# Kernel tuning notes

Measured on AMD Instinct MI355X. Metric: run time of the kernel, lower is better.

The kernel has to match this reference:

```python
import jax, jax.numpy as jnp
import numpy as np

B, T, D_IN, H = 128, 256, 512, 1024

def setup_inputs() -> dict:
    key = jax.random.key(0)
    ks = jax.random.split(key, 12)
    s = 1.0 / np.sqrt(H)
    return {
        "input": jax.random.normal(ks[0], (B, T, D_IN), jnp.float32),
        "h0": jax.random.normal(ks[1], (B, H), jnp.float32),
        "c0": jax.random.normal(ks[2], (B, H), jnp.float32),
        "ctx": jax.random.normal(ks[3], (B, T, H), jnp.float32),
        "srcmask": jax.random.randint(ks[4], (B, T), 0, 2).astype(bool),
        "W_ih": jax.random.uniform(ks[5], (4 * H, D_IN), jnp.float32, -s, s),
        "W_hh": jax.random.uniform(ks[6], (4 * H, H), jnp.float32, -s, s),
        "b_ih": jax.random.uniform(ks[7], (4 * H,), jnp.float32, -s, s),
        "b_hh": jax.random.uniform(ks[8], (4 * H,), jnp.float32, -s, s),
        "W_attn": jax.random.uniform(ks[9], (H, H), jnp.float32, -s, s),
        "W_out": jax.random.uniform(ks[10], (H, 2 * H), jnp.float32, -s, s),
    }


def reference(input, h0, c0, ctx, srcmask, W_ih, W_hh, b_ih, b_hh, W_attn, W_out):
    def step(carry, x_t):
        h, c = carry
        # LSTMCell: gate order i, f, g, o (PyTorch convention)
        gates = x_t @ W_ih.T + b_ih + h @ W_hh.T + b_hh  # [B, 4H]
        i_g, f_g, g_g, o_g = jnp.split(gates, 4, axis=-1)
        cy = jax.nn.sigmoid(f_g) * c + jax.nn.sigmoid(i_g) * jnp.tanh(g_g)
        hy = jax.nn.sigmoid(o_g) * jnp.tanh(cy)
        # Bilinear attention: score(K_j, q) = K_j^T (W_attn q)
        q = hy @ W_attn.T                                   # [B, H]
        scores = jnp.einsum("blh,bh->bl", ctx, q)          # [B, L]
        scores = jnp.where(srcmask, -jnp.inf, scores)
        probs = jax.nn.softmax(scores, axis=-1)
        wctx = jnp.einsum("bl,blh->bh", probs, ctx)        # [B, H]
        h_tilde = jnp.tanh(jnp.concatenate([wctx, hy], axis=-1) @ W_out.T)
        return (h_tilde, cy), h_tilde

    xs = jnp.transpose(input, (1, 0, 2))  # [T, B, D_IN]
    (h_f, c_f), outs = jax.lax.scan(step, (h0, c0), xs)
    output = jnp.transpose(outs, (1, 0, 2))  # [B, T, H]
    return (output, h_f, c_f)
```

## Files before the change

kernel.cpp:

```cpp
#include <hip/hip_runtime.h>
#include <hip/hip_bf16.h>
#include <math.h>

#define B_  128
#define T_  256
#define DIN 512
#define H_  1024

typedef __attribute__((ext_vector_type(8))) short bf16x8;
typedef __attribute__((ext_vector_type(4))) float f32x4;

#define GLD_LDS16(gsrc, ldst) \
  __builtin_amdgcn_global_load_lds((const __attribute__((address_space(1))) void*)(gsrc), \
                                   (__attribute__((address_space(3))) void*)(ldst), 16, 0, 0)

#define WAITVM_(n) asm volatile("s_waitcnt vmcnt(" #n ")" ::: "memory")
#define WAITVM(n) WAITVM_(n)

__device__ __forceinline__ void split_bf16(float v, __hip_bfloat16* hi, __hip_bfloat16* lo) {
    __hip_bfloat16 h = __float2bfloat16(v);
    *hi = h;
    *lo = __float2bfloat16(v - __bfloat162float(h));
}

__device__ __forceinline__ float sigmoidf_(float x) { return 1.f / (1.f + expf(-x)); }

__global__ void bsum_perm_k(const float* __restrict__ bi, const float* __restrict__ bh,
                            float* __restrict__ o) {
    int c = blockIdx.x * 256 + threadIdx.x;
    int srow = ((c & 3) << 10) | (c >> 2);
    o[c] = bi[srow] + bh[srow];
}

__global__ void detect_mask_k(const int* __restrict__ m, int nwords, int* __restrict__ flag) {
    __shared__ int bad;
    if (threadIdx.x == 0) bad = 0;
    __syncthreads();
    for (int i = threadIdx.x; i < nwords; i += blockDim.x) {
        unsigned v = (unsigned)m[i];
        if (v > 1u) bad = 1;
    }
    __syncthreads();
    if (threadIdx.x == 0) flag[0] = bad ? 0 : 1;
}

__global__ void cvt_split_k(const float* __restrict__ s, __hip_bfloat16* __restrict__ hi,
                            __hip_bfloat16* __restrict__ lo, int n) {
    int i = blockIdx.x * 256 + threadIdx.x;
    if (i < n) split_bf16(s[i], hi + i, lo + i);
}

__global__ void wgp_split_k(const float* __restrict__ Wih, const float* __restrict__ Whh,
                            __hip_bfloat16* __restrict__ Wh, __hip_bfloat16* __restrict__ Wl) {
    long i = (long)blockIdx.x * 256 + threadIdx.x;
    int c = (int)(i / 1536), k = (int)(i - (long)c * 1536);
    int srow = ((c & 3) << 10) | (c >> 2);
    float v = (k < DIN) ? Wih[(long)srow * DIN + k] : Whh[(long)srow * H_ + (k - DIN)];
    split_bf16(v, Wh + i, Wl + i);
}

__global__ void cvtx_k(const float* __restrict__ xsrc, __hip_bfloat16* __restrict__ xh,
                       __hip_bfloat16* __restrict__ xl) {
    int i = blockIdx.x * 256 + threadIdx.x;
    int b = i >> 9, c = i & 511;
    split_bf16(xsrc[(long)b * (T_ * DIN) + c], xh + i, xl + i);
}

constexpr int APL = 128 * 64 * 2;
constexpr int BPL = 32 * 64 * 2;
constexpr int BUFB = 2 * APL + 2 * BPL;
constexpr int LDSZ = 3 * BUFB;

#define GEMM_CORE(NT, NW2, BNV, VMID, NB, KSP, A1H, A1L, LDA1, K1V, A2H, A2L, LDA2, WHP, WLP, LDW) \
    const int n0_ = (NB) * (BNV); \
    const int kbase_ = (KSP) * ((NT) * 64); \
    const int wm_ = (NW2) ? (w >> 1) * 64 : w * 32; \
    const int wn_ = (NW2) ? (w & 1) * 16 : 0; \
    auto stage = [&](int buf, int kt) { \
        char* base = lds + buf * BUFB; \
        const int kb = kbase_ + kt * 64; \
        _Pragma("unroll") \
        for (int pp = 0; pp < 2; ++pp) { \
            const __hip_bfloat16* A1 = pp ? (A1L) : (A1H); \
            const __hip_bfloat16* A2 = pp ? (A2L) : (A2H); \
            _Pragma("unroll") \
            for (int j = 0; j < 4; ++j) { \
                int c = j * 256 + tid; \
                int row = c >> 3, sl2 = c & 7; \
                int e = kb + ((sl2 ^ (row & 7)) << 3); \
                const __hip_bfloat16* src = (e < (K1V)) ? (A1 + (long)row * (LDA1) + e) \
                                                        : (A2 + (long)row * (LDA2) + (e - (K1V))); \
                GLD_LDS16(src, base + pp * APL + ((j * 256 + (tid & 192)) << 4)); \
            } \
            if (tid < (BNV) * 8) { \
                int row = tid >> 3, sl2 = tid & 7; \
                int e = kb + ((sl2 ^ (row & 7)) << 3); \
                const __hip_bfloat16* src = (pp ? (WLP) : (WHP)) + (long)(n0_ + row) * (LDW) + e; \
                GLD_LDS16(src, base + 2 * APL + pp * BPL + ((tid & 192) << 4)); \
            } \
        } \
    }; \
    f32x4 acc[4] = {}; \
    stage(0, 0); \
    if ((NT) > 1) stage(1, 1); \
    for (int kt = 0; kt < (NT); ++kt) { \
        if (kt + 1 < (NT)) { WAITVM(VMID); } else { WAITVM(0); } \
        __builtin_amdgcn_s_barrier(); \
        __builtin_amdgcn_sched_barrier(0); \
        if (kt + 2 < (NT)) stage((kt + 2) % 3, kt + 2); \
        const char* base = lds + (kt % 3) * BUFB; \
        _Pragma("unroll") \
        for (int ks = 0; ks < 2; ++ks) { \
            bf16x8 afh[4], afl[4], bh, bl; \
            _Pragma("unroll") \
            for (int mi = 0; mi < ((NW2) ? 4 : 2); ++mi) { \
                int row = wm_ + mi * 16 + (l & 15); \
                int sl2 = (l >> 4) + ks * 4; \
                int off = row * 128 + ((sl2 ^ (row & 7)) << 4); \
                afh[mi] = *(const bf16x8*)(base + off); \
                afl[mi] = *(const bf16x8*)(base + APL + off); \
            } \
            { \
                int row = wn_ + (l & 15); \
                int sl2 = (l >> 4) + ks * 4; \
                int off = row * 128 + ((sl2 ^ (row & 7)) << 4); \
                bh = *(const bf16x8*)(base + 2 * APL + off); \
                bl = *(const bf16x8*)(base + 2 * APL + BPL + off); \
            } \
            _Pragma("unroll") \
            for (int mi = 0; mi < ((NW2) ? 4 : 2); ++mi) { \
                acc[mi] = __builtin_amdgcn_mfma_f32_16x16x32_bf16(afh[mi], bh, acc[mi], 0, 0, 0); \
                acc[mi] = __builtin_amdgcn_mfma_f32_16x16x32_bf16(afl[mi], bh, acc[mi], 0, 0, 0); \
                acc[mi] = __builtin_amdgcn_mfma_f32_16x16x32_bf16(afh[mi], bl, acc[mi], 0, 0, 0); \
            } \
        } \
    }

__global__ __launch_bounds__(256)
void gemm_g_k(const __hip_bfloat16* __restrict__ xh, const __hip_bfloat16* __restrict__ xl,
              const __hip_bfloat16* __restrict__ hh, const __hip_bfloat16* __restrict__ hl,
              const __hip_bfloat16* __restrict__ Wgh, const __hip_bfloat16* __restrict__ Wgl,
              const float* __restrict__ bsump, float* __restrict__ cbuf,
              __hip_bfloat16* __restrict__ AoBh, __hip_bfloat16* __restrict__ AoBl,
              float* __restrict__ cf,
              const float* __restrict__ input, int t,
              __hip_bfloat16* __restrict__ nxh, __hip_bfloat16* __restrict__ nxl)
{
    __shared__ __attribute__((aligned(16))) char lds[LDSZ];
    const int blk = blockIdx.x, tid = threadIdx.x;
    const int l = tid & 63, w = tid >> 6;

    GEMM_CORE(24, 1, 32, 10, blk, 0,
              xh, xl, DIN, DIN, hh, hl, H_, Wgh, Wgl, (DIN + H_));

    __syncthreads();
    float* sg = (float*)lds;
    {
        float bv = bsump[n0_ + wn_ + (l & 15)];
        #pragma unroll
        for (int mi = 0; mi < 4; ++mi) {
            int rbase = wm_ + mi * 16 + (l >> 4) * 4;
            int col = wn_ + (l & 15);
            #pragma unroll
            for (int r = 0; r < 4; ++r)
                sg[(rbase + r) * 36 + col] = acc[mi][r] + bv;
        }
    }
    __syncthreads();

    #pragma unroll
    for (int k = 0; k < 4; ++k) {
        int ci = k * 256 + tid;
        int b = ci >> 3, jp = ci & 7;
        float4 g4 = *(const float4*)&sg[b * 36 + jp * 4];
        int j = blk * 8 + jp;
        long idx = (long)b * H_ + j;
        float ig = sigmoidf_(g4.x);
        float fg = sigmoidf_(g4.y);
        float gg = tanhf(g4.z);
        float og = sigmoidf_(g4.w);
        float c = fg * cbuf[idx] + ig * gg;
        float h = og * tanhf(c);
        cbuf[idx] = c;
        split_bf16(h, AoBh + (long)b * 2048 + 1024 + j, AoBl + (long)b * 2048 + 1024 + j);
        if (cf) cf[idx] = c;
    }

    if (t + 1 < T_) {
        #pragma unroll
        for (int k = 0; k < 2; ++k) {
            int i2 = blk * 512 + k * 256 + tid;
            int b2 = i2 >> 9, col = i2 & 511;
            float v = input[((long)b2 * T_ + (t + 1)) * DIN + col];
            split_bf16(v, nxh + i2, nxl + i2);
        }
    }
}

__global__ __launch_bounds__(256)
void gemm_q_k(const __hip_bfloat16* __restrict__ AoBh, const __hip_bfloat16* __restrict__ AoBl,
              const __hip_bfloat16* __restrict__ Wah, const __hip_bfloat16* __restrict__ Wal,
              float* __restrict__ qpart)
{
    __shared__ __attribute__((aligned(16))) char lds[LDSZ];
    const int tid = threadIdx.x;
    const int l = tid & 63, w = tid >> 6;

    GEMM_CORE(4, 1, 32, 10, (int)blockIdx.x, (int)blockIdx.y,
              (AoBh + H_), (AoBl + H_), (2 * H_), H_,
              (AoBh + H_), (AoBl + H_), (2 * H_), Wah, Wal, H_);

    float* Cb = qpart + (long)blockIdx.y * (B_ * H_);
    const int n = n0_ + wn_ + (l & 15);
    #pragma unroll
    for (int mi = 0; mi < 4; ++mi) {
        int mbase = wm_ + mi * 16 + (l >> 4) * 4;
        #pragma unroll
        for (int r = 0; r < 4; ++r)
            Cb[(long)(mbase + r) * H_ + n] = acc[mi][r];
    }
}

__global__ __launch_bounds__(256)
void attn_k(const float* __restrict__ ctx, const float* __restrict__ qpart,
            const void* __restrict__ maskp, const int* __restrict__ mflag,
            __hip_bfloat16* __restrict__ AoBh, __hip_bfloat16* __restrict__ AoBl)
{
    constexpr int L = T_, H = H_;
    __shared__ float sacc[4][H_];
    __shared__ float sms[4][2];
    int b = blockIdx.x;
    const float* cb = ctx + (long)b * L * H;
    int tid = threadIdx.x, l = tid & 63, w = tid >> 6;
    int mode = mflag[0];

    float rq[16];
    #pragma unroll
    for (int j = 0; j < 16; ++j) {
        long o = (long)b * H + l + j * 64;
        rq[j] = qpart[o] + qpart[o + 131072] + qpart[o + 262144] + qpart[o + 393216];
    }

    float m = -INFINITY, s = 0.f, acc[16] = {};
    for (int li = w; li < L; li += 4) {
        bool msk = mode ? (((const int*)maskp)[b * L + li] != 0)
                        : (((const unsigned char*)maskp)[b * L + li] != 0);
        if (msk) continue;
        const float* cr = cb + (long)li * H;
        float rc[16], d = 0.f;
        #pragma unroll
        for (int j = 0; j < 16; ++j) { rc[j] = cr[l + j * 64]; d += rc[j] * rq[j]; }
        #pragma unroll
        for (int off = 1; off < 64; off <<= 1) d += __shfl_xor(d, off);
        float mn = fmaxf(m, d);
        float f = expf(m - mn);
        float p = expf(d - mn);
        s = s * f + p;
        #pragma unroll
        for (int j = 0; j < 16; ++j) acc[j] = acc[j] * f + p * rc[j];
        m = mn;
    }

    #pragma unroll
    for (int j = 0; j < 16; ++j) sacc[w][l + j * 64] = acc[j];
    if (l == 0) { sms[w][0] = m; sms[w][1] = s; }
    __syncthreads();

    float M = fmaxf(fmaxf(sms[0][0], sms[1][0]), fmaxf(sms[2][0], sms[3][0]));
    float fw[4], S = 0.f;
    #pragma unroll
    for (int ww = 0; ww < 4; ++ww) {
        fw[ww] = (sms[ww][0] == -INFINITY) ? 0.f : expf(sms[ww][0] - M);
        S += fw[ww] * sms[ww][1];
    }
    float inv = 1.f / S;
    for (int k = tid; k < H; k += 256) {
        float a = sacc[0][k] * fw[0] + sacc[1][k] * fw[1] + sacc[2][k] * fw[2] + sacc[3][k] * fw[3];
        split_bf16(a * inv, AoBh + (long)b * 2048 + k, AoBl + (long)b * 2048 + k);
    }
}

__global__ __launch_bounds__(256)
void gemm_o_k(const __hip_bfloat16* __restrict__ AoBh, const __hip_bfloat16* __restrict__ AoBl,
              const __hip_bfloat16* __restrict__ Woh, const __hip_bfloat16* __restrict__ Wol,
              __hip_bfloat16* __restrict__ hth, __hip_bfloat16* __restrict__ htl,
              float* __restrict__ out, int t, float* __restrict__ hf)
{
    __shared__ __attribute__((aligned(16))) char lds[LDSZ];
    const int tid = threadIdx.x;
    const int l = tid & 63, w = tid >> 6;

    GEMM_CORE(32, 0, 16, 8, (int)blockIdx.x, 0,
              AoBh, AoBl, (2 * H_), (2 * H_),
              AoBh, AoBl, (2 * H_), Woh, Wol, (2 * H_));

    const int j = n0_ + (l & 15);
    #pragma unroll
    for (int mi = 0; mi < 2; ++mi) {
        int bbase = wm_ + mi * 16 + (l >> 4) * 4;
        #pragma unroll
        for (int r = 0; r < 4; ++r) {
            int b = bbase + r;
            float v = tanhf(acc[mi][r]);
            split_bf16(v, hth + (long)b * H_ + j, htl + (long)b * H_ + j);
            out[(long)b * (T_ * H_) + (long)t * H_ + j] = v;
            if (hf) hf[(long)b * H_ + j] = v;
        }
    }
}

extern "C" void kernel_launch(void* const* d_in, const int* in_sizes, int n_in,
                              void* d_out, int out_size, void* d_ws, size_t ws_size,
                              hipStream_t stream)
{
    const float* input  = (const float*)d_in[0];
    const float* h0     = (const float*)d_in[1];
    const float* c0     = (const float*)d_in[2];
    const float* ctx    = (const float*)d_in[3];
    const void*  srcmask= d_in[4];
    const float* W_ih   = (const float*)d_in[5];
    const float* W_hh   = (const float*)d_in[6];
    const float* b_ih   = (const float*)d_in[7];
    const float* b_hh   = (const float*)d_in[8];
    const float* W_attn = (const float*)d_in[9];
    const float* W_out  = (const float*)d_in[10];

    constexpr int B = B_, T = T_, D = DIN, H = H_;

    float* f = (float*)d_ws;
    float* bsump = f; f += 4 * H;
    float* cbuf  = f; f += (size_t)B * H;
    float* qpart = f; f += (size_t)4 * B * H;
    int*   mflag = (int*)f; f += 64;
    __hip_bfloat16* p = (__hip_bfloat16*)f;
    __hip_bfloat16* Wgh = p; p += (size_t)4 * H * (D + H);
    __hip_bfloat16* Wgl = p; p += (size_t)4 * H * (D + H);
    __hip_bfloat16* Wah = p; p += (size_t)H * H;
    __hip_bfloat16* Wal = p; p += (size_t)H * H;
    __hip_bfloat16* Woh = p; p += (size_t)H * 2 * H;
    __hip_bfloat16* Wol = p; p += (size_t)H * 2 * H;
    __hip_bfloat16* hth = p; p += (size_t)B * H;
    __hip_bfloat16* htl = p; p += (size_t)B * H;
    __hip_bfloat16* AoBh = p; p += (size_t)B * 2 * H;
    __hip_bfloat16* AoBl = p; p += (size_t)B * 2 * H;
    __hip_bfloat16* xth[2], *xtl[2];
    xth[0] = p; p += (size_t)B * D;
    xtl[0] = p; p += (size_t)B * D;
    xth[1] = p; p += (size_t)B * D;
    xtl[1] = p; p += (size_t)B * D;

    float* out = (float*)d_out;
    float* hf  = out + (size_t)B * T * H;
    float* cf  = hf + (size_t)B * H;

    hipMemcpyAsync(cbuf, c0, (size_t)B * H * sizeof(float), hipMemcpyDeviceToDevice, stream);
    bsum_perm_k<<<dim3(16), dim3(256), 0, stream>>>(b_ih, b_hh, bsump);
    detect_mask_k<<<dim3(1), dim3(256), 0, stream>>>((const int*)srcmask, B * T / 4, mflag);
    wgp_split_k<<<dim3(4 * H * (D + H) / 256), dim3(256), 0, stream>>>(W_ih, W_hh, Wgh, Wgl);
    cvt_split_k<<<dim3(H * H / 256), dim3(256), 0, stream>>>(W_attn, Wah, Wal, H * H);
    cvt_split_k<<<dim3(H * 2 * H / 256), dim3(256), 0, stream>>>(W_out, Woh, Wol, H * 2 * H);
    cvt_split_k<<<dim3(B * H / 256), dim3(256), 0, stream>>>(h0, hth, htl, B * H);
    cvtx_k<<<dim3(B * D / 256), dim3(256), 0, stream>>>(input, xth[0], xtl[0]);

    dim3 blk(256);
    for (int t = 0; t < T; ++t) {
        int sl = t & 1, sn = sl ^ 1;

        gemm_g_k<<<dim3(128), blk, 0, stream>>>(
            xth[sl], xtl[sl], hth, htl, Wgh, Wgl, bsump, cbuf,
            AoBh, AoBl, (t == T - 1) ? cf : nullptr,
            input, t, xth[sn], xtl[sn]);

        gemm_q_k<<<dim3(32, 4), blk, 0, stream>>>(AoBh, AoBl, Wah, Wal, qpart);

        attn_k<<<dim3(B), blk, 0, stream>>>(ctx, qpart, srcmask, mflag, AoBh, AoBl);

        gemm_o_k<<<dim3(64), blk, 0, stream>>>(
            AoBh, AoBl, Woh, Wol, hth, htl, out, t, (t == T - 1) ? hf : nullptr);
    }
}
```

Baseline: 21.53 ms.

## Fuse per-step kernels into two launches with inter-block flag synchronization

Cuts the four kernels per timestep down to two. Each merged kernel splits its blocks into roles that talk through global atomic counters and cache-bypassing (sc0 sc1) loads and stores. The gate GEMM is split-K across 256 blocks, and the spare blocks go on to the attention-query GEMM once all h values are published. The output GEMM is split into four K partitions, partly overlapped with the attention blocks and reduced through a partial buffer. The aim is to cut launch overhead and fill more CUs, at the cost of spin-waits that assume every block is co-resident, plus extra partial-sum traffic.

```diff
diff --git a/kernel.cpp b/kernel.cpp
--- a/kernel.cpp
+++ b/kernel.cpp
@@ -14,9 +14,6 @@
   __builtin_amdgcn_global_load_lds((const __attribute__((address_space(1))) void*)(gsrc), \
                                    (__attribute__((address_space(3))) void*)(ldst), 16, 0, 0)
 
-#define WAITVM_(n) asm volatile("s_waitcnt vmcnt(" #n ")" ::: "memory")
-#define WAITVM(n) WAITVM_(n)
-
 __device__ __forceinline__ void split_bf16(float v, __hip_bfloat16* hi, __hip_bfloat16* lo) {
     __hip_bfloat16 h = __float2bfloat16(v);
     *hi = h;
@@ -24,6 +21,27 @@
 }
 
 __device__ __forceinline__ float sigmoidf_(float x) { return 1.f / (1.f + expf(-x)); }
+
+__device__ __forceinline__ void cohld1_issue(float* dst, const float* ptr) {
+    asm volatile("global_load_dword %0, %1, off sc0 sc1" : "=v"(*dst) : "v"(ptr));
+}
+__device__ __forceinline__ void cohst1(float* ptr, float v) {
+    asm volatile("global_store_dword %0, %1, off sc0 sc1" :: "v"(ptr), "v"(v) : "memory");
+}
+__device__ __forceinline__ void cohst_u16(unsigned short* ptr, unsigned int v) {
+    asm volatile("global_store_short %0, %1, off sc0 sc1" :: "v"(ptr), "v"(v) : "memory");
+}
+__device__ __forceinline__ void cohst_split(unsigned short* hip_, unsigned short* lop_, float v) {
+    __hip_bfloat16 h, lo2;
+    split_bf16(v, &h, &lo2);
+    cohst_u16(hip_, *(unsigned short*)&h);
+    cohst_u16(lop_, *(unsigned short*)&lo2);
+}
+#define COH_WAIT() do { asm volatile("s_waitcnt vmcnt(0)" ::: "memory"); \
+                        __builtin_amdgcn_sched_barrier(0); } while (0)
+
+#define AADD(pp) __hip_atomic_fetch_add((pp), 1u, __ATOMIC_RELAXED, __HIP_MEMORY_SCOPE_AGENT)
+#define ALOAD(pp) __hip_atomic_load((pp), __ATOMIC_RELAXED, __HIP_MEMORY_SCOPE_AGENT)
 
 __global__ void bsum_perm_k(const float* __restrict__ bi, const float* __restrict__ bh,
                             float* __restrict__ o) {
@@ -71,11 +89,10 @@
 constexpr int BUFB = 2 * APL + 2 * BPL;
 constexpr int LDSZ = 3 * BUFB;
 
-#define GEMM_CORE(NT, NW2, BNV, VMID, NB, KSP, A1H, A1L, LDA1, K1V, A2H, A2L, LDA2, WHP, WLP, LDW) \
-    const int n0_ = (NB) * (BNV); \
+#define GEMM_CORE(NT, NB, KSP, A1H, A1L, LDA1, K1V, A2H, A2L, LDA2, WHP, WLP, LDW) \
+    const int n0_ = (NB) * 32; \
     const int kbase_ = (KSP) * ((NT) * 64); \
-    const int wm_ = (NW2) ? (w >> 1) * 64 : w * 32; \
-    const int wn_ = (NW2) ? (w & 1) * 16 : 0; \
+    const int wm_ = (w >> 1) * 64, wn_ = (w & 1) * 16; \
     auto stage = [&](int buf, int kt) { \
         char* base = lds + buf * BUFB; \
         const int kb = kbase_ + kt * 64; \
@@ -92,7 +109,7 @@
                                                         : (A2 + (long)row * (LDA2) + (e - (K1V))); \
                 GLD_LDS16(src, base + pp * APL + ((j * 256 + (tid & 192)) << 4)); \
             } \
-            if (tid < (BNV) * 8) { \
+            { \
                 int row = tid >> 3, sl2 = tid & 7; \
                 int e = kb + ((sl2 ^ (row & 7)) << 3); \
                 const __hip_bfloat16* src = (pp ? (WLP) : (WHP)) + (long)(n0_ + row) * (LDW) + e; \
@@ -104,7 +121,8 @@
     stage(0, 0); \
     if ((NT) > 1) stage(1, 1); \
     for (int kt = 0; kt < (NT); ++kt) { \
-        if (kt + 1 < (NT)) { WAITVM(VMID); } else { WAITVM(0); } \
+        if (kt + 1 < (NT)) asm volatile("s_waitcnt vmcnt(10)" ::: "memory"); \
+        else               asm volatile("s_waitcnt vmcnt(0)"  ::: "memory"); \
         __builtin_amdgcn_s_barrier(); \
         __builtin_amdgcn_sched_barrier(0); \
         if (kt + 2 < (NT)) stage((kt + 2) % 3, kt + 2); \
@@ -113,7 +131,7 @@
         for (int ks = 0; ks < 2; ++ks) { \
             bf16x8 afh[4], afl[4], bh, bl; \
             _Pragma("unroll") \
-            for (int mi = 0; mi < ((NW2) ? 4 : 2); ++mi) { \
+            for (int mi = 0; mi < 4; ++mi) { \
                 int row = wm_ + mi * 16 + (l & 15); \
                 int sl2 = (l >> 4) + ks * 4; \
                 int off = row * 128 + ((sl2 ^ (row & 7)) << 4); \
@@ -128,7 +146,7 @@
                 bl = *(const bf16x8*)(base + 2 * APL + BPL + off); \
             } \
             _Pragma("unroll") \
-            for (int mi = 0; mi < ((NW2) ? 4 : 2); ++mi) { \
+            for (int mi = 0; mi < 4; ++mi) { \
                 acc[mi] = __builtin_amdgcn_mfma_f32_16x16x32_bf16(afh[mi], bh, acc[mi], 0, 0, 0); \
                 acc[mi] = __builtin_amdgcn_mfma_f32_16x16x32_bf16(afl[mi], bh, acc[mi], 0, 0, 0); \
                 acc[mi] = __builtin_amdgcn_mfma_f32_16x16x32_bf16(afh[mi], bl, acc[mi], 0, 0, 0); \
@@ -136,175 +154,346 @@
         } \
     }
 
+#define GEMM_CORE_COH(NT, NB, KSP, AH, AL, LDA, WHP, WLP, LDW) \
+    const int n0_ = (NB) * 32; \
+    const int kbase_ = (KSP) * ((NT) * 64); \
+    const int wm_ = (w >> 1) * 64, wn_ = (w & 1) * 16; \
+    uint4 rA[2][4]; \
+    auto issueA = [&](int kt) { \
+        const int kb = kbase_ + kt * 64; \
+        _Pragma("unroll") \
+        for (int pp = 0; pp < 2; ++pp) { \
+            const unsigned short* Ap = (const unsigned short*)(pp ? (AL) : (AH)); \
+            _Pragma("unroll") \
+            for (int j = 0; j < 4; ++j) { \
+                int c = j * 256 + tid; \
+                int row = c >> 3, sl2 = c & 7; \
+                int e = kb + ((sl2 ^ (row & 7)) << 3); \
+                const unsigned short* src = Ap + (long)row * (LDA) + e; \
+                asm volatile("global_load_dwordx4 %0, %1, off sc0 sc1" \
+                             : "=v"(rA[pp][j]) : "v"(src)); \
+            } \
+        } \
+    }; \
+    auto writeA = [&](int buf) { \
+        char* wb = lds + buf * BUFB; \
+        _Pragma("unroll") \
+        for (int pp = 0; pp < 2; ++pp) \
+            _Pragma("unroll") \
+            for (int j = 0; j < 4; ++j) \
+                *(uint4*)(wb + pp * APL + (j * 256 + tid) * 16) = rA[pp][j]; \
+    }; \
+    auto issueB = [&](int kt, int buf) { \
+        char* bb = lds + buf * BUFB; \
+        const int kb = kbase_ + kt * 64; \
+        int row = tid >> 3, sl2 = tid & 7; \
+        int e = kb + ((sl2 ^ (row & 7)) << 3); \
+        _Pragma("unroll") \
+        for (int pp = 0; pp < 2; ++pp) { \
+            const __hip_bfloat16* src = (pp ? (WLP) : (WHP)) + (long)(n0_ + row) * (LDW) + e; \
+            GLD_LDS16(src, bb + 2 * APL + pp * BPL + ((tid & 192) << 4)); \
+        } \
+    }; \
+    f32x4 acc[4] = {}; \
+    issueA(0); issueB(0, 0); \
+    asm volatile("s_waitcnt vmcnt(2)" ::: "memory"); \
+    __builtin_amdgcn_sched_barrier(0); \
+    writeA(0); \
+    issueA(1); issueB(1, 1); \
+    for (int kt = 0; kt < (NT); ++kt) { \
+        asm volatile("s_waitcnt vmcnt(0) lgkmcnt(0)" ::: "memory"); \
+        __builtin_amdgcn_s_barrier(); \
+        __builtin_amdgcn_sched_barrier(0); \
+        if (kt + 1 < (NT)) writeA((kt + 1) % 3); \
+        if (kt + 2 < (NT)) { issueA(kt + 2); issueB(kt + 2, (kt + 2) % 3); } \
+        const char* base = lds + (kt % 3) * BUFB; \
+        _Pragma("unroll") \
+        for (int ks = 0; ks < 2; ++ks) { \
+            bf16x8 afh[4], afl[4], bh, bl; \
+            _Pragma("unroll") \
+            for (int mi = 0; mi < 4; ++mi) { \
+                int row = wm_ + mi * 16 + (l & 15); \
+                int sl2 = (l >> 4) + ks * 4; \
+                int off = row * 128 + ((sl2 ^ (row & 7)) << 4); \
+                afh[mi] = *(const bf16x8*)(base + off); \
+                afl[mi] = *(const bf16x8*)(base + APL + off); \
+            } \
+            { \
+                int row = wn_ + (l & 15); \
+                int sl2 = (l >> 4) + ks * 4; \
+                int off = row * 128 + ((sl2 ^ (row & 7)) << 4); \
+                bh = *(const bf16x8*)(base + 2 * APL + off); \
+                bl = *(const bf16x8*)(base + 2 * APL + BPL + off); \
+            } \
+            _Pragma("unroll") \
+            for (int mi = 0; mi < 4; ++mi) { \
+                acc[mi] = __builtin_amdgcn_mfma_f32_16x16x32_bf16(afh[mi], bh, acc[mi], 0, 0, 0); \
+                acc[mi] = __builtin_amdgcn_mfma_f32_16x16x32_bf16(afl[mi], bh, acc[mi], 0, 0, 0); \
+                acc[mi] = __builtin_amdgcn_mfma_f32_16x16x32_bf16(afh[mi], bl, acc[mi], 0, 0, 0); \
+            } \
+        } \
+    }
+
 __global__ __launch_bounds__(256)
-void gemm_g_k(const __hip_bfloat16* __restrict__ xh, const __hip_bfloat16* __restrict__ xl,
-              const __hip_bfloat16* __restrict__ hh, const __hip_bfloat16* __restrict__ hl,
-              const __hip_bfloat16* __restrict__ Wgh, const __hip_bfloat16* __restrict__ Wgl,
-              const float* __restrict__ bsump, float* __restrict__ cbuf,
-              __hip_bfloat16* __restrict__ AoBh, __hip_bfloat16* __restrict__ AoBl,
-              float* __restrict__ cf,
-              const float* __restrict__ input, int t,
-              __hip_bfloat16* __restrict__ nxh, __hip_bfloat16* __restrict__ nxl)
+void node1_k(const __hip_bfloat16* __restrict__ xh, const __hip_bfloat16* __restrict__ xl,
+             const __hip_bfloat16* __restrict__ hh, const __hip_bfloat16* __restrict__ hl,
+             const __hip_bfloat16* __restrict__ Wgh, const __hip_bfloat16* __restrict__ Wgl,
+             const __hip_bfloat16* __restrict__ Wah, const __hip_bfloat16* __restrict__ Wal,
+             const float* __restrict__ bsump, float* __restrict__ cbuf,
+             unsigned short* __restrict__ AoBh, unsigned short* __restrict__ AoBl,
+             float* __restrict__ gpart, float* __restrict__ qpart,
+             unsigned* __restrict__ gflag, unsigned* __restrict__ hcnt,
+             float* __restrict__ cf,
+             const float* __restrict__ input, int t,
+             __hip_bfloat16* __restrict__ nxh, __hip_bfloat16* __restrict__ nxl)
 {
     __shared__ __attribute__((aligned(16))) char lds[LDSZ];
     const int blk = blockIdx.x, tid = threadIdx.x;
     const int l = tid & 63, w = tid >> 6;
 
-    GEMM_CORE(24, 1, 32, 10, blk, 0,
-              xh, xl, DIN, DIN, hh, hl, H_, Wgh, Wgl, (DIN + H_));
-
-    __syncthreads();
-    float* sg = (float*)lds;
-    {
-        float bv = bsump[n0_ + wn_ + (l & 15)];
+    if (blk < 128) {
+        const int ct = blk;
+        GEMM_CORE(12, ct, 0, xh, xl, DIN, DIN, hh, hl, H_, Wgh, Wgl, (DIN + H_));
+
+        if (tid == 0) while (ALOAD(&gflag[t * 128 + ct]) < 1u) __builtin_amdgcn_s_sleep(2);
+        __syncthreads();
+
+        float pv[4][4];
         #pragma unroll
         for (int mi = 0; mi < 4; ++mi) {
-            int rbase = wm_ + mi * 16 + (l >> 4) * 4;
+            int rb = wm_ + mi * 16 + (l >> 4) * 4;
             int col = wn_ + (l & 15);
             #pragma unroll
             for (int r = 0; r < 4; ++r)
-                sg[(rbase + r) * 36 + col] = acc[mi][r] + bv;
+                cohld1_issue(&pv[mi][r], gpart + ct * 4096 + (rb + r) * 32 + col);
+        }
+        COH_WAIT();
+
+        float* sg = (float*)lds;
+        {
+            float bv = bsump[n0_ + wn_ + (l & 15)];
+            #pragma unroll
+            for (int mi = 0; mi < 4; ++mi) {
+                int rb = wm_ + mi * 16 + (l >> 4) * 4;
+                int col = wn_ + (l & 15);
+                #pragma unroll
+                for (int r = 0; r < 4; ++r)
+                    sg[(rb + r) * 36 + col] = acc[mi][r] + pv[mi][r] + bv;
+            }
+        }
+        __syncthreads();
+
+        #pragma unroll
+        for (int k = 0; k < 4; ++k) {
+            int ci = k * 256 + tid;
+            int b = ci >> 3, jp = ci & 7;
+            float4 g4 = *(const float4*)&sg[b * 36 + jp * 4];
+            int j = ct * 8 + jp;
+            long idx = (long)b * H_ + j;
+            float ig = sigmoidf_(g4.x);
+            float fg = sigmoidf_(g4.y);
+            float gg = tanhf(g4.z);
+            float og = sigmoidf_(g4.w);
+            float c = fg * cbuf[idx] + ig * gg;
+            float h = og * tanhf(c);
+            cbuf[idx] = c;
+            cohst_split(AoBh + (long)b * 2048 + 1024 + j,
+                        AoBl + (long)b * 2048 + 1024 + j, h);
+            if (cf) cf[idx] = c;
+        }
+        COH_WAIT();
+        __syncthreads();
+        if (tid == 0) AADD(&hcnt[t]);
+
+        if (t + 1 < T_) {
+            #pragma unroll
+            for (int k = 0; k < 2; ++k) {
+                int i2 = blk * 512 + k * 256 + tid;
+                int b2 = i2 >> 9, col = i2 & 511;
+                float v = input[((long)b2 * T_ + (t + 1)) * DIN + col];
+                split_bf16(v, nxh + i2, nxl + i2);
+            }
+        }
+    } else {
+        const int ct = blk - 128;
+        {
+            GEMM_CORE(12, ct, 1, xh, xl, DIN, DIN, hh, hl, H_, Wgh, Wgl, (DIN + H_));
+            #pragma unroll
+            for (int mi = 0; mi < 4; ++mi) {
+                int rb = wm_ + mi * 16 + (l >> 4) * 4;
+                int col = wn_ + (l & 15);
+                #pragma unroll
+                for (int r = 0; r < 4; ++r)
+                    cohst1(gpart + ct * 4096 + (rb + r) * 32 + col, acc[mi][r]);
+            }
+            COH_WAIT();
+            __syncthreads();
+            if (tid == 0) AADD(&gflag[t * 128 + ct]);
+        }
+
+        if (tid == 0) while (ALOAD(&hcnt[t]) < 128u) __builtin_amdgcn_s_sleep(2);
+        __syncthreads();
+        {
+            const int qct = ct & 31, qksp = ct >> 5;
+            GEMM_CORE_COH(4, qct, qksp,
+                          ((const unsigned short*)AoBh + H_), ((const unsigned short*)AoBl + H_),
+                          (2 * H_), Wah, Wal, H_);
+            float* Cb = qpart + (long)qksp * (B_ * H_);
+            const int n = n0_ + wn_ + (l & 15);
+            #pragma unroll
+            for (int mi = 0; mi < 4; ++mi) {
+                int rb = wm_ + mi * 16 + (l >> 4) * 4;
+                #pragma unroll
+                for (int r = 0; r < 4; ++r)
+                    Cb[(long)(rb + r) * H_ + n] = acc[mi][r];
+            }
         }
     }
-    __syncthreads();
-
-    #pragma unroll
-    for (int k = 0; k < 4; ++k) {
-        int ci = k * 256 + tid;
-        int b = ci >> 3, jp = ci & 7;
-        float4 g4 = *(const float4*)&sg[b * 36 + jp * 4];
-        int j = blk * 8 + jp;
-        long idx = (long)b * H_ + j;
-        float ig = sigmoidf_(g4.x);
-        float fg = sigmoidf_(g4.y);
-        float gg = tanhf(g4.z);
-        float og = sigmoidf_(g4.w);
-        float c = fg * cbuf[idx] + ig * gg;
-        float h = og * tanhf(c);
-        cbuf[idx] = c;
-        split_bf16(h, AoBh + (long)b * 2048 + 1024 + j, AoBl + (long)b * 2048 + 1024 + j);
-        if (cf) cf[idx] = c;
-    }
-
-    if (t + 1 < T_) {
-        #pragma unroll
-        for (int k = 0; k < 2; ++k) {
-            int i2 = blk * 512 + k * 256 + tid;
-            int b2 = i2 >> 9, col = i2 & 511;
-            float v = input[((long)b2 * T_ + (t + 1)) * DIN + col];
-            split_bf16(v, nxh + i2, nxl + i2);
-        }
-    }
 }
 
 __global__ __launch_bounds__(256)
-void gemm_q_k(const __hip_bfloat16* __restrict__ AoBh, const __hip_bfloat16* __restrict__ AoBl,
-              const __hip_bfloat16* __restrict__ Wah, const __hip_bfloat16* __restrict__ Wal,
-              float* __restrict__ qpart)
+void node2_k(const float* __restrict__ ctx, const float* __restrict__ qpart,
+             const void* __restrict__ maskp, const int* __restrict__ mflag,
+             const __hip_bfloat16* __restrict__ Woh, const __hip_bfloat16* __restrict__ Wol,
+             unsigned short* __restrict__ AoBh, unsigned short* __restrict__ AoBl,
+             float* __restrict__ opart,
+             unsigned* __restrict__ wcnt, unsigned* __restrict__ ocnt,
+             __hip_bfloat16* __restrict__ hth, __hip_bfloat16* __restrict__ htl,
+             float* __restrict__ out, int t, float* __restrict__ hf)
 {
     __shared__ __attribute__((aligned(16))) char lds[LDSZ];
-    const int tid = threadIdx.x;
+    const int blk = blockIdx.x, tid = threadIdx.x;
     const int l = tid & 63, w = tid >> 6;
 
-    GEMM_CORE(4, 1, 32, 10, (int)blockIdx.x, (int)blockIdx.y,
-              (AoBh + H_), (AoBl + H_), (2 * H_), H_,
-              (AoBh + H_), (AoBl + H_), (2 * H_), Wah, Wal, H_);
-
-    float* Cb = qpart + (long)blockIdx.y * (B_ * H_);
-    const int n = n0_ + wn_ + (l & 15);
-    #pragma unroll
-    for (int mi = 0; mi < 4; ++mi) {
-        int mbase = wm_ + mi * 16 + (l >> 4) * 4;
+    if (blk < 128) {
+        const int b = blk;
+        const float* cb = ctx + (long)b * (T_ * H_);
+        const int mode = mflag[0];
+
+        float rq[16];
         #pragma unroll
-        for (int r = 0; r < 4; ++r)
-            Cb[(long)(mbase + r) * H_ + n] = acc[mi][r];
-    }
-}
-
-__global__ __launch_bounds__(256)
-void attn_k(const float* __restrict__ ctx, const float* __restrict__ qpart,
-            const void* __restrict__ maskp, const int* __restrict__ mflag,
-            __hip_bfloat16* __restrict__ AoBh, __hip_bfloat16* __restrict__ AoBl)
-{
-    constexpr int L = T_, H = H_;
-    __shared__ float sacc[4][H_];
-    __shared__ float sms[4][2];
-    int b = blockIdx.x;
-    const float* cb = ctx + (long)b * L * H;
-    int tid = threadIdx.x, l = tid & 63, w = tid >> 6;
-    int mode = mflag[0];
-
-    float rq[16];
-    #pragma unroll
-    for (int j = 0; j < 16; ++j) {
-        long o = (long)b * H + l + j * 64;
-        rq[j] = qpart[o] + qpart[o + 131072] + qpart[o + 262144] + qpart[o + 393216];
-    }
-
-    float m = -INFINITY, s = 0.f, acc[16] = {};
-    for (int li = w; li < L; li += 4) {
-        bool msk = mode ? (((const int*)maskp)[b * L + li] != 0)
-                        : (((const unsigned char*)maskp)[b * L + li] != 0);
-        if (msk) continue;
-        const float* cr = cb + (long)li * H;
-        float rc[16], d = 0.f;
+        for (int j = 0; j < 16; ++j) {
+            long o = (long)b * H_ + l * 16 + j;
+            rq[j] = qpart[o] + qpart[o + 131072] + qpart[o + 262144] + qpart[o + 393216];
+        }
+
+        float m = -INFINITY, s = 0.f, acc[16] = {};
+        for (int li = w; li < T_; li += 4) {
+            bool msk = mode ? (((const int*)maskp)[b * T_ + li] != 0)
+                            : (((const unsigned char*)maskp)[b * T_ + li] != 0);
+            if (msk) continue;
+            const float4* cr4 = (const float4*)(cb + (long)li * H_ + l * 16);
+            float4 v0 = cr4[0], v1 = cr4[1], v2 = cr4[2], v3 = cr4[3];
+            float rc[16] = { v0.x, v0.y, v0.z, v0.w, v1.x, v1.y, v1.z, v1.w,
+                             v2.x, v2.y, v2.z, v2.w, v3.x, v3.y, v3.z, v3.w };
+            float d = 0.f;
+            #pragma unroll
+            for (int j = 0; j < 16; ++j) d += rc[j] * rq[j];
+            #pragma unroll
+            for (int off = 1; off < 64; off <<= 1) d += __shfl_xor(d, off);
+            float mn = fmaxf(m, d);
+            float f = expf(m - mn);
+            float pp = expf(d - mn);
+            s = s * f + pp;
+            #pragma unroll
+            for (int j = 0; j < 16; ++j) acc[j] = acc[j] * f + pp * rc[j];
+            m = mn;
+        }
+
+        float (*sacc)[H_] = (float (*)[H_])lds;
+        float (*sms)[2] = (float (*)[2])(lds + 4 * H_ * sizeof(float));
         #pragma unroll
-        for (int j = 0; j < 16; ++j) { rc[j] = cr[l + j * 64]; d += rc[j] * rq[j]; }
+        for (int j = 0; j < 16; ++j) sacc[w][l * 16 + j] = acc[j];
+        if (l == 0) { sms[w][0] = m; sms[w][1] = s; }
+        __syncthreads();
+
+        float M = fmaxf(fmaxf(sms[0][0], sms[1][0]), fmaxf(sms[2][0], sms[3][0]));
+        float fw[4], S = 0.f;
         #pragma unroll
-        for (int off = 1; off < 64; off <<= 1) d += __shfl_xor(d, off);
-        float mn = fmaxf(m, d);
-        float f = expf(m - mn);
-        float p = expf(d - mn);
-        s = s * f + p;
-        #pragma unroll
-        for (int j = 0; j < 16; ++j) acc[j] = acc[j] * f + p * rc[j];
-        m = mn;
-    }
-
-    #pragma unroll
-    for (int j = 0; j < 16; ++j) sacc[w][l + j * 64] = acc[j];
-    if (l == 0) { sms[w][0] = m; sms[w][1] = s; }
-    __syncthreads();
-
-    float M = fmaxf(fmaxf(sms[0][0], sms[1][0]), fmaxf(sms[2][0], sms[3][0]));
-    float fw[4], S = 0.f;
-    #pragma unroll
-    for (int ww = 0; ww < 4; ++ww) {
-        fw[ww] = (sms[ww][0] == -INFINITY) ? 0.f : expf(sms[ww][0] - M);
-        S += fw[ww] * sms[ww][1];
-    }
-    float inv = 1.f / S;
-    for (int k = tid; k < H; k += 256) {
-        float a = sacc[0][k] * fw[0] + sacc[1][k] * fw[1] + sacc[2][k] * fw[2] + sacc[3][k] * fw[3];
-        split_bf16(a * inv, AoBh + (long)b * 2048 + k, AoBl + (long)b * 2048 + k);
-    }
-}
-
-__global__ __launch_bounds__(256)
-void gemm_o_k(const __hip_bfloat16* __restrict__ AoBh, const __hip_bfloat16* __restrict__ AoBl,
-              const __hip_bfloat16* __restrict__ Woh, const __hip_bfloat16* __restrict__ Wol,
-              __hip_bfloat16* __restrict__ hth, __hip_bfloat16* __restrict__ htl,
-              float* __restrict__ out, int t, float* __restrict__ hf)
-{
-    __shared__ __attribute__((aligned(16))) char lds[LDSZ];
-    const int tid = threadIdx.x;
-    const int l = tid & 63, w = tid >> 6;
-
-    GEMM_CORE(32, 0, 16, 8, (int)blockIdx.x, 0,
-              AoBh, AoBl, (2 * H_), (2 * H_),
-              AoBh, AoBl, (2 * H_), Woh, Wol, (2 * H_));
-
-    const int j = n0_ + (l & 15);
-    #pragma unroll
-    for (int mi = 0; mi < 2; ++mi) {
-        int bbase = wm_ + mi * 16 + (l >> 4) * 4;
-        #pragma unroll
-        for (int r = 0; r < 4; ++r) {
-            int b = bbase + r;
-            float v = tanhf(acc[mi][r]);
-            split_bf16(v, hth + (long)b * H_ + j, htl + (long)b * H_ + j);
-            out[(long)b * (T_ * H_) + (long)t * H_ + j] = v;
-            if (hf) hf[(long)b * H_ + j] = v;
+        for (int ww = 0; ww < 4; ++ww) {
+            fw[ww] = (sms[ww][0] == -INFINITY) ? 0.f : expf(sms[ww][0] - M);
+            S += fw[ww] * sms[ww][1];
+        }
+        float inv = 1.f / S;
+        for (int k = tid; k < H_; k += 256) {
+            float a = (sacc[0][k] * fw[0] + sacc[1][k] * fw[1] +
+                       sacc[2][k] * fw[2] + sacc[3][k] * fw[3]) * inv;
+            cohst_split(AoBh + (long)b * 2048 + k, AoBl + (long)b * 2048 + k, a);
+        }
+        COH_WAIT();
+        __syncthreads();
+        if (tid == 0) AADD(&wcnt[t]);
+    } else {
+        const int idx = blk - 128;
+        const int ct = idx & 31, ksp = idx >> 5;
+
+        if (ksp >= 2) {
+            GEMM_CORE(8, ct, ksp,
+                      (const __hip_bfloat16*)AoBh, (const __hip_bfloat16*)AoBl,
+                      (2 * H_), (4 * H_),
+                      (const __hip_bfloat16*)AoBh, (const __hip_bfloat16*)AoBl, (2 * H_),
+                      Woh, Wol, (2 * H_));
+            #pragma unroll
+            for (int mi = 0; mi < 4; ++mi) {
+                int rb = wm_ + mi * 16 + (l >> 4) * 4;
+                int col = wn_ + (l & 15);
+                #pragma unroll
+                for (int r = 0; r < 4; ++r)
+                    cohst1(opart + (long)(ksp - 1) * 131072 + ct * 4096 + (rb + r) * 32 + col,
+                           acc[mi][r]);
+            }
+            COH_WAIT();
+            __syncthreads();
+            if (tid == 0) AADD(&ocnt[t * 32 + ct]);
+        } else {
+            if (tid == 0) while (ALOAD(&wcnt[t]) < 128u) __builtin_amdgcn_s_sleep(2);
+            __syncthreads();
+            GEMM_CORE_COH(8, ct, ksp,
+                          (const unsigned short*)AoBh, (const unsigned short*)AoBl,
+                          (2 * H_), Woh, Wol, (2 * H_));
+            if (ksp == 1) {
+                #pragma unroll
+                for (int mi = 0; mi < 4; ++mi) {
+                    int rb = wm_ + mi * 16 + (l >> 4) * 4;
+                    int col = wn_ + (l & 15);
+                    #pragma unroll
+                    for (int r = 0; r < 4; ++r)
+                        cohst1(opart + ct * 4096 + (rb + r) * 32 + col, acc[mi][r]);
+                }
+                COH_WAIT();
+                __syncthreads();
+                if (tid == 0) AADD(&ocnt[t * 32 + ct]);
+            } else {
+                if (tid == 0) while (ALOAD(&ocnt[t * 32 + ct]) < 3u) __builtin_amdgcn_s_sleep(2);
+                __syncthreads();
+                float pv[3][4][4];
+                #pragma unroll
+                for (int q = 0; q < 3; ++q)
+                    #pragma unroll
+                    for (int mi = 0; mi < 4; ++mi) {
+                        int rb = wm_ + mi * 16 + (l >> 4) * 4;
+                        int col = wn_ + (l & 15);
+                        #pragma unroll
+                        for (int r = 0; r < 4; ++r)
+                            cohld1_issue(&pv[q][mi][r],
+                                opart + (long)q * 131072 + ct * 4096 + (rb + r) * 32 + col);
+                    }
+                COH_WAIT();
+                const int j = n0_ + wn_ + (l & 15);
+                #pragma unroll
+                for (int mi = 0; mi < 4; ++mi) {
+                    int rb = wm_ + mi * 16 + (l >> 4) * 4;
+                    #pragma unroll
+                    for (int r = 0; r < 4; ++r) {
+                        int b = rb + r;
+                        float v = acc[mi][r] + pv[0][mi][r] + pv[1][mi][r] + pv[2][mi][r];
+                        v = tanhf(v);
+                        split_bf16(v, hth + (long)b * H_ + j, htl + (long)b * H_ + j);
+                        out[(long)b * (T_ * H_) + (long)t * H_ + j] = v;
+                        if (hf) hf[(long)b * H_ + j] = v;
+                    }
+                }
+            }
         }
     }
 }
@@ -330,8 +519,14 @@
     float* f = (float*)d_ws;
     float* bsump = f; f += 4 * H;
     float* cbuf  = f; f += (size_t)B * H;
+    float* gpart = f; f += (size_t)128 * 4096;
     float* qpart = f; f += (size_t)4 * B * H;
+    float* opart = f; f += (size_t)3 * 32 * 4096;
     int*   mflag = (int*)f; f += 64;
+    unsigned* gflag = (unsigned*)f; f += 32768;
+    unsigned* hcnt  = (unsigned*)f; f += 256;
+    unsigned* wcnt  = (unsigned*)f; f += 256;
+    unsigned* ocnt  = (unsigned*)f; f += 8192;
     __hip_bfloat16* p = (__hip_bfloat16*)f;
     __hip_bfloat16* Wgh = p; p += (size_t)4 * H * (D + H);
     __hip_bfloat16* Wgl = p; p += (size_t)4 * H * (D + H);
@@ -353,6 +548,7 @@
     float* hf  = out + (size_t)B * T * H;
     float* cf  = hf + (size_t)B * H;
 
+    hipMemsetAsync(gflag, 0, (32768 + 256 + 256 + 8192) * sizeof(unsigned), stream);
     hipMemcpyAsync(cbuf, c0, (size_t)B * H * sizeof(float), hipMemcpyDeviceToDevice, stream);
     bsum_perm_k<<<dim3(16), dim3(256), 0, stream>>>(b_ih, b_hh, bsump);
     detect_mask_k<<<dim3(1), dim3(256), 0, stream>>>((const int*)srcmask, B * T / 4, mflag);
@@ -366,16 +562,17 @@
     for (int t = 0; t < T; ++t) {
         int sl = t & 1, sn = sl ^ 1;
 
-        gemm_g_k<<<dim3(128), blk, 0, stream>>>(
-            xth[sl], xtl[sl], hth, htl, Wgh, Wgl, bsump, cbuf,
-            AoBh, AoBl, (t == T - 1) ? cf : nullptr,
+        node1_k<<<dim3(256), blk, 0, stream>>>(
+            xth[sl], xtl[sl], hth, htl, Wgh, Wgl, Wah, Wal, bsump, cbuf,
+            (unsigned short*)AoBh, (unsigned short*)AoBl,
+            gpart, qpart, gflag, hcnt,
+            (t == T - 1) ? cf : nullptr,
             input, t, xth[sn], xtl[sn]);
 
-        gemm_q_k<<<dim3(32, 4), blk, 0, stream>>>(AoBh, AoBl, Wah, Wal, qpart);
-
-        attn_k<<<dim3(B), blk, 0, stream>>>(ctx, qpart, srcmask, mflag, AoBh, AoBl);
-
-        gemm_o_k<<<dim3(64), blk, 0, stream>>>(
-            AoBh, AoBl, Woh, Wol, hth, htl, out, t, (t == T - 1) ? hf : nullptr);
+        node2_k<<<dim3(256), blk, 0, stream>>>(
+            ctx, qpart, srcmask, mflag, Woh, Wol,
+            (unsigned short*)AoBh, (unsigned short*)AoBl,
+            opart, wcnt, ocnt, hth, htl,
+            out, t, (t == T - 1) ? hf : nullptr);
     }
 }
```

New measurement: 21.60 ms. Within noise of the previous version (+0.3%).
